# Optimization experiments

Hardware: AMD Instinct MI355X
Metric: run time of the kernel (lower is better)

Reference implementation:

```python
import jax, jax.numpy as jnp
import numpy as np

THRESH = 1.0
TAU_M = 20.0
TAU_S = 5.0
NUM_STEPS = 8
SCALE = 0.2
BATCH = 8
DM = np.float32(np.exp(-1.0 / TAU_M))
DS = np.float32(np.exp(-1.0 / TAU_S))


@jax.custom_vjp
def spike_fn(x):
    return (x > 0.0).astype(x.dtype)

def _sf_fwd(x):
    return (x > 0.0).astype(x.dtype), x

def _sf_bwd(x, g):
    # rectangular surrogate gradient (lens = 0.5), standard for NOSO/SNN training
    return (g * (jnp.abs(x) < 0.5).astype(x.dtype),)

spike_fn.defvjp(_sf_fwd, _sf_bwd)


def conv5x5(x, w):
    return jax.lax.conv_general_dilated(x, w, (1, 1), ((2, 2), (2, 2)),
                                        dimension_numbers=('NCHW', 'OIHW', 'NCHW'))


def noso_conv(w, in_sp, sav, vm, vs):
    # dual-exponential NOSO neuron: pre-synaptic traces vm/vs, membrane u = sav*(conv(vm)-conv(vs))
    vm = DM * vm + in_sp
    vs = DS * vs + in_sp
    um = conv5x5(vm, w)
    us = conv5x5(vs, w)
    u = sav * (um - us)
    sp = spike_fn(u - THRESH)
    sav = sav * (1.0 - sp)  # one spike per neuron
    return sav, vm, vs, um, u, sp


def noso_fc(w, in_sp, sav, vm, vs):
    vm = DM * vm + in_sp
    vs = DS * vs + in_sp
    um = jnp.einsum('bi,oi->bo', vm, w)
    us = jnp.einsum('bi,oi->bo', vs, w)
    u = sav * (um - us)
    sp = spike_fn(u - THRESH)
    sav = sav * (1.0 - sp)
    return sav, vm, vs, um, u, sp


def minpool(sp, lat):
    # latency-based 2x2 min-pool: pass through the spike whose neuron fired earliest
    b, c, h, w = sp.shape
    s = sp.reshape(b, c, h // 2, 2, w // 2, 2).transpose(0, 1, 2, 4, 3, 5).reshape(b, c, h // 2, w // 2, 4)
    l = lat.reshape(b, c, h // 2, 2, w // 2, 2).transpose(0, 1, 2, 4, 3, 5).reshape(b, c, h // 2, w // 2, 4)
    idx = jnp.argmin(l, axis=-1)
    return jnp.take_along_axis(s, idx[..., None], axis=-1)[..., 0]


def xavier(key, shape, fan_in, fan_out):
    a = np.float32(np.sqrt(6.0 / (fan_in + fan_out)))
    return jax.random.uniform(key, shape, jnp.float32, -a, a)


def setup_inputs():
    key = jax.random.key(0)
    ks = jax.random.split(key, 9)
    inp = {'input': jax.random.uniform(ks[0], (BATCH, 3, 32, 32), jnp.float32)}
    def cw(k, o, i):
        return xavier(k, (o, i, 5, 5), i * 25, o * 25)
    def lw(k, o, i):
        return xavier(k, (o, i), i, o)
    inp['wc1'] = cw(ks[1], 64, 3)
    inp['wc2'] = cw(ks[2], 128, 64)
    inp['wc3'] = cw(ks[3], 256, 128)
    inp['wc4'] = cw(ks[4], 512, 256)
    inp['wc5'] = cw(ks[5], 256, 512)
    inp['wf1'] = lw(ks[6], 1024, 16384)
    inp['wf2'] = lw(ks[7], 512, 1024)
    inp['wf3'] = lw(ks[8], 10, 512)
    inp['batch_size'] = BATCH
    return inp


def forward(input, wc1, wc2, wc3, wc4, wc5, wf1, wf2, wf3, batch_size):
    B = batch_size
    f32 = jnp.float32
    def Z(*s):
        return jnp.zeros((B,) + s, f32)
    def O(*s):
        return jnp.ones((B,) + s, f32)
    carry = {
        'in_u': Z(3, 32, 32),
        'h1': (O(64, 32, 32), Z(3, 32, 32), Z(3, 32, 32)),
        'h2': (O(128, 32, 32), Z(64, 32, 32), Z(64, 32, 32)),
        'h3': (O(256, 16, 16), Z(128, 16, 16), Z(128, 16, 16)),
        'h4': (O(512, 8, 8), Z(256, 8, 8), Z(256, 8, 8)),
        'h5': (O(256, 8, 8), Z(512, 8, 8), Z(512, 8, 8)),
        'f1': (O(1024), Z(16384), Z(16384)),
        'f2': (O(512), Z(1024), Z(1024)),
        'f3': (O(10), Z(512), Z(512)),
        'p1e': Z(128, 32, 32),
        'p1l': float(NUM_STEPS) * O(128, 32, 32),
        'p2e': Z(256, 16, 16),
        'p2l': float(NUM_STEPS) * O(256, 16, 16),
        'te': Z(10),
        'out_t': float(NUM_STEPS) * O(10),
        'out_u': Z(10),
        'sum_sp': jnp.zeros((9,), f32),
    }

    def step(c, _):
        # input encoding neuron (thresh=1, leaky integrate + reset on spike)
        in_u = DM * c['in_u'] + input * SCALE
        in_sp = spike_fn(in_u - 1.0)
        in_u = in_u * (1.0 - in_sp)
        s1, vm1, vs1, um1, u1, sp1 = noso_conv(wc1, in_sp, *c['h1'])
        s2, vm2, vs2, um2, u2, sp2 = noso_conv(wc2, sp1, *c['h2'])
        p1e = c['p1e'] + ((c['p1e'] + (um2 != 0).astype(f32)) != 0).astype(f32)
        p1l = c['p1l'] + jax.lax.stop_gradient(sp2) * (p1e - NUM_STEPS + 1.0)
        s3, vm3, vs3, um3, u3, sp3 = noso_conv(wc3, minpool(sp2, p1l), *c['h3'])
        p2e = c['p2e'] + ((c['p2e'] + (um3 != 0).astype(f32)) != 0).astype(f32)
        p2l = c['p2l'] + jax.lax.stop_gradient(sp3) * (p2e - NUM_STEPS + 1.0)
        s4, vm4, vs4, um4, u4, sp4 = noso_conv(wc4, minpool(sp3, p2l), *c['h4'])
        s5, vm5, vs5, um5, u5, sp5 = noso_conv(wc5, sp4, *c['h5'])
        sf1, vmf1, vsf1, umf1, uf1, spf1 = noso_fc(wf1, sp5.reshape(B, -1), *c['f1'])
        sf2, vmf2, vsf2, umf2, uf2, spf2 = noso_fc(wf2, spf1, *c['f2'])
        sf3, vmf3, vsf3, umf3, uf3, spf3 = noso_fc(wf3, spf2, *c['f3'])
        te = c['te'] + ((c['te'] + (uf3 != 0).astype(f32)) != 0).astype(f32)
        out_t = c['out_t'] + spf3 * jax.lax.stop_gradient(te - NUM_STEPS)  # dodt forward
        out_u = c['out_u'] + spf3 * uf3
        sum_sp = c['sum_sp'] + jnp.stack([in_sp.sum(), sp1.sum(), sp2.sum(), sp3.sum(),
                                          sp4.sum(), sp5.sum(), spf1.sum(), spf2.sum(), spf3.sum()])
        nc = {'in_u': in_u,
              'h1': (s1, vm1, vs1), 'h2': (s2, vm2, vs2), 'h3': (s3, vm3, vs3),
              'h4': (s4, vm4, vs4), 'h5': (s5, vm5, vs5),
              'f1': (sf1, vmf1, vsf1), 'f2': (sf2, vmf2, vsf2), 'f3': (sf3, vmf3, vsf3),
              'p1e': p1e, 'p1l': p1l, 'p2e': p2e, 'p2l': p2l,
              'te': te, 'out_t': out_t, 'out_u': out_u, 'sum_sp': sum_sp}
        return nc, None

    c, _ = jax.lax.scan(step, carry, None, length=NUM_STEPS)
    return c['out_t'], c['out_u'], c['sum_sp']


def reference(input, wc1, wc2, wc3, wc4, wc5, wf1, wf2, wf3, batch_size):
    return forward(input, wc1, wc2, wc3, wc4, wc5, wf1, wf2, wf3, batch_size)
```

## Files before the change

kernel.cpp:

```cpp
#include <hip/hip_runtime.h>
#include <cstddef>

#define B 8
constexpr int TAIL_NB = 256;

constexpr float DM = 0.95122942450071400910f;
constexpr float DS = 0.81873075307798185867f;

constexpr int BS_L0 = 3 * 32 * 32;
constexpr int BS_L1 = 64 * 32 * 32;
constexpr int BS_P1 = 128 * 16 * 16;
constexpr int BS_P2 = 256 * 8 * 8;
constexpr int BS_L4 = 512 * 8 * 8;
constexpr int BS_L5 = 256 * 8 * 8;
constexpr int BS_F1 = 1024;
constexpr int BS_F2 = 512;

constexpr size_t I_L1 = 0;
constexpr size_t I_P1 = I_L1 + 8 * (size_t)B * BS_L1;
constexpr size_t I_P2 = I_P1 + 8 * (size_t)B * BS_P1;
constexpr size_t I_L4 = I_P2 + 8 * (size_t)B * BS_P2;
constexpr size_t I_L5 = I_L4 + 8 * (size_t)B * BS_L4;
constexpr size_t I_F1 = I_L5 + 8 * (size_t)B * BS_L5;
constexpr size_t I_F2 = I_F1 + 8 * (size_t)B * BS_F1;
constexpr size_t I_CNT = I_F2 + 8 * (size_t)B * BS_F2;
constexpr size_t I_SUMP = I_CNT + 512;
constexpr size_t I_BAR = I_SUMP + 16;
constexpr size_t INT_TOTAL = I_BAR + 2;
constexpr size_t WS_NEED = INT_TOTAL * sizeof(int);

constexpr int ilog2(int n) { int l = 0; while (n > 1) { n >>= 1; ++l; } return l; }

__device__ __forceinline__ int ldcnt(const int* p) {
  return __hip_atomic_load(p, __ATOMIC_RELAXED, __HIP_MEMORY_SCOPE_AGENT);
}

__device__ __forceinline__ void block_stage(bool sp, int idx, int* s_list, int* s_n) {
  unsigned long long bal = __ballot(sp);
  if (bal == 0ull) return;
  int lane = threadIdx.x & 63;
  int leader = (int)__ffsll((unsigned long long)bal) - 1;
  int base = 0;
  if (lane == leader) base = atomicAdd(s_n, __popcll(bal));
  base = __shfl(base, leader);
  if (sp) s_list[base + __popcll(bal & ((1ull << lane) - 1ull))] = idx;
}

__device__ __forceinline__ void wave_append(bool sp, int idx, int* cnt, int* list) {
  unsigned long long bal = __ballot(sp);
  if (bal == 0ull) return;
  int lane = threadIdx.x & 63;
  int leader = (int)__ffsll((unsigned long long)bal) - 1;
  int base = 0;
  if (lane == leader) base = atomicAdd(cnt, __popcll(bal));
  base = __shfl(base, leader);
  if (sp) list[base + __popcll(bal & ((1ull << lane) - 1ull))] = idx;
}

__device__ __forceinline__ bool layer_any(const int* cnt, int ci, int tid, int* s_gate) {
  __syncthreads();
  if (tid == 0) *s_gate = 0;
  __syncthreads();
  if (tid < 64) {
    int t = tid >> 3, b = tid & 7;
    if (ldcnt(cnt + (t * 8 + ci) * 8 + b) > 0) *s_gate = 1;
  }
  __syncthreads();
  return *s_gate != 0;
}

__device__ __forceinline__ void gbar(int* bar, int tid) {
  __threadfence();
  __syncthreads();
  if (tid == 0) {
    int g = __hip_atomic_load(bar + 1, __ATOMIC_RELAXED, __HIP_MEMORY_SCOPE_AGENT);
    int a = __hip_atomic_fetch_add(bar, 1, __ATOMIC_ACQ_REL, __HIP_MEMORY_SCOPE_AGENT);
    if (a == TAIL_NB - 1) {
      __hip_atomic_store(bar, 0, __ATOMIC_RELAXED, __HIP_MEMORY_SCOPE_AGENT);
      __hip_atomic_store(bar + 1, g + 1, __ATOMIC_RELEASE, __HIP_MEMORY_SCOPE_AGENT);
    } else {
      while (__hip_atomic_load(bar + 1, __ATOMIC_ACQUIRE, __HIP_MEMORY_SCOPE_AGENT) == g)
        __builtin_amdgcn_s_sleep(1);
    }
  }
  __syncthreads();
  __threadfence();
}

__global__ void k_init(int* __restrict__ cw) {
  if (threadIdx.x < 530) cw[threadIdx.x] = 0;
}

__global__ __launch_bounds__(512) void k_conv1_enc(const float* __restrict__ in,
                                                   const float* __restrict__ w,
                                                   int* __restrict__ cnt,
                                                   int* __restrict__ out_list0) {
  const int tid = threadIdx.x;
  const int plane = blockIdx.x;
  const int b = plane >> 6;
  const int oc = plane & 63;
  __shared__ float s_w[75];
  __shared__ float s_acc[1024];
  __shared__ int s_list[BS_L0];
  __shared__ int s_n;
  if (tid < 75) s_w[tid] = w[oc * 75 + tid];
  float x[6], u[6];
#pragma unroll
  for (int k = 0; k < 6; ++k) {
    x[k] = in[b * BS_L0 + tid + k * 512] * 0.2f;
    u[k] = 0.0f;
  }
  float um[2], us[2], sav[2];
#pragma unroll
  for (int k = 0; k < 2; ++k) { um[k] = 0.0f; us[k] = 0.0f; sav[k] = 1.0f; }
  bool active = false;
#pragma clang loop unroll(disable)
  for (int t = 0; t < 8; ++t) {
    if (tid == 0) s_n = 0;
    __syncthreads();
#pragma unroll
    for (int k = 0; k < 6; ++k) {
      u[k] = DM * u[k] + x[k];
      bool sp = (u[k] - 1.0f > 0.0f);
      if (sp) u[k] = 0.0f;
      block_stage(sp, tid + k * 512, s_list, &s_n);
    }
    __syncthreads();
    const int Sin = s_n;
    if (oc == 0 && tid == 0) cnt[(t * 8 + 0) * 8 + b] = Sin;
    active = active || (Sin > 0);
    if (!active) continue;
#pragma clang loop unroll(disable)
    for (int p = tid; p < 1024; p += 512) s_acc[p] = 0.0f;
    __syncthreads();
    const int total = Sin << 5;
#pragma clang loop unroll(disable)
    for (int i = tid; i < total; i += 512) {
      int k = i & 31;
      if (k < 25) {
        int loc = s_list[i >> 5];
        int c = loc >> 10;
        int p = loc & 1023;
        int ki = (k * 205) >> 10;
        int oy = (p >> 5) + 2 - ki;
        int ox = (p & 31) + 2 - (k - ki * 5);
        if ((unsigned)oy < 32u && (unsigned)ox < 32u)
          atomicAdd(&s_acc[(oy << 5) + ox], s_w[c * 25 + k]);
      }
    }
    __syncthreads();
    int* out_cnt = cnt + (t * 8 + 1) * 8 + b;
    int* out_list = out_list0 + ((size_t)t * B + b) * BS_L1;
#pragma unroll
    for (int k = 0; k < 2; ++k) {
      int p = tid + k * 512;
      float cv = s_acc[p];
      float m = DM * um[k] + cv;
      float s2 = DS * us[k] + cv;
      um[k] = m;
      us[k] = s2;
      float uu = sav[k] * (m - s2);
      bool sp = (uu - 1.0f > 0.0f);
      if (sp) sav[k] = 0.0f;
      wave_append(sp, (oc << 10) + p, out_cnt, out_list);
    }
    __syncthreads();
  }
}

template <int CIN, int COUT, int H, int W, bool POOL, int PPB, bool WLDS>
__device__ void conv_phase(int bid, int tid, const float* __restrict__ w, int* cnt, int in_ci,
                           int out_ci, const int* __restrict__ in_list0, int in_bs,
                           int* __restrict__ out_list0, int out_bs, float* sump_layer,
                           float* s_acc, float* s_plb, float* s_spb, float* s_w, int* s_list,
                           int* s_n, int* s_base, int* s_uc, int* s_cnt) {
  constexpr int HW = H * W;
  constexpr int HWlog = ilog2(HW);
  constexpr int Wlog = ilog2(W);
  constexpr int PPT = (HW + 255) / 256;
  int wcount = 0;
  const int b = (bid * PPB) >> ilog2(COUT);
  if (tid < 8) s_cnt[tid] = ldcnt(cnt + (tid * 8 + in_ci) * 8 + b);
  __syncthreads();
#pragma clang loop unroll(disable)
  for (int pl = 0; pl < PPB; ++pl) {
    const int plane = bid * PPB + pl;
    const int oc = plane & (COUT - 1);
    if constexpr (WLDS) {
#pragma clang loop unroll(disable)
      for (int j = tid; j < CIN * 25; j += 256) s_w[j] = w[(size_t)oc * CIN * 25 + j];
    }
    float um[PPT], us[PPT], sav[PPT], pe[PPT], plat[PPT];
#pragma unroll
    for (int k = 0; k < PPT; ++k) {
      um[k] = 0.0f; us[k] = 0.0f; sav[k] = 1.0f; pe[k] = 0.0f; plat[k] = 8.0f;
    }
    bool active = false;
#pragma clang loop unroll(disable)
    for (int t = 0; t < 8; ++t) {
      const int S = s_cnt[t];
      if (!active && S == 0) continue;
      active = true;
#pragma clang loop unroll(disable)
      for (int p = tid; p < HW; p += 256) s_acc[p] = 0.0f;
      if (tid == 0) *s_n = 0;
      __syncthreads();
      const int* list = in_list0 + ((size_t)t * B + b) * in_bs;
#pragma clang loop unroll(disable)
      for (int s = tid; s < S; s += 256) {
        int loc = list[s];
        int c = loc >> HWlog;
        int p = loc & (HW - 1);
        int y = p >> Wlog, x = p & (W - 1);
        const float* wp = WLDS ? (const float*)s_w + c * 25 : w + ((size_t)oc * CIN + c) * 25;
#pragma clang loop unroll(disable)
        for (int ki = 0; ki < 5; ++ki) {
          int oy = y + 2 - ki;
          if ((unsigned)oy < (unsigned)H) {
#pragma clang loop unroll(disable)
            for (int kj = 0; kj < 5; ++kj) {
              int ox = x + 2 - kj;
              if ((unsigned)ox < (unsigned)W) atomicAdd(&s_acc[oy * W + ox], wp[ki * 5 + kj]);
            }
          }
        }
      }
      __syncthreads();
#pragma unroll
      for (int k = 0; k < PPT; ++k) {
        int p = tid + k * 256;
        bool lane_ok = (p < HW);
        float cv = lane_ok ? s_acc[p] : 0.0f;
        float m = DM * um[k] + cv;
        float s2 = DS * us[k] + cv;
        um[k] = m;
        us[k] = s2;
        float uu = sav[k] * (m - s2);
        bool sp = lane_ok && (uu - 1.0f > 0.0f);
        if (sp) sav[k] = 0.0f;
        if constexpr (POOL) {
          unsigned long long bal = __ballot(sp);
          if ((tid & 63) == 0) wcount += (int)__popcll(bal);
          if (lane_ok) {
            float act = (m != 0.0f) ? 1.0f : 0.0f;
            float pen = pe[k] + (((pe[k] + act) != 0.0f) ? 1.0f : 0.0f);
            pe[k] = pen;
            if (sp) plat[k] += pen - 7.0f;
            s_plb[p] = plat[k];
            s_spb[p] = sp ? 1.0f : 0.0f;
          }
        } else {
          block_stage(sp, (oc << HWlog) + p, s_list, s_n);
        }
      }
      __syncthreads();
      if constexpr (POOL) {
        constexpr int HP = H / 2, WP = W / 2;
#pragma clang loop unroll(disable)
        for (int q = tid; q < HP * WP; q += 256) {
          int py = q / WP, px = q - py * WP;
          int base = (2 * py) * W + 2 * px;
          float l0 = s_plb[base], l1 = s_plb[base + 1], l2 = s_plb[base + W],
                l3 = s_plb[base + W + 1];
          int off = 0;
          float lm = l0;
          if (l1 < lm) { lm = l1; off = 1; }
          if (l2 < lm) { lm = l2; off = W; }
          if (l3 < lm) { lm = l3; off = W + 1; }
          bool psp = (s_spb[base + off] != 0.0f);
          block_stage(psp, oc * (HP * WP) + q, s_list, s_n);
        }
        __syncthreads();
      }
      if (tid == 0 && *s_n > 0) *s_base = atomicAdd(cnt + (t * 8 + out_ci) * 8 + b, *s_n);
      __syncthreads();
      int* out_list = out_list0 + ((size_t)t * B + b) * out_bs;
      int n = *s_n;
#pragma clang loop unroll(disable)
      for (int j = tid; j < n; j += 256) out_list[*s_base + j] = s_list[j];
      __syncthreads();
    }
  }
  if constexpr (POOL) {
    if (tid == 0) *s_uc = 0;
    __syncthreads();
    if ((tid & 63) == 0 && wcount) atomicAdd(s_uc, wcount);
    __syncthreads();
    if (tid == 0 && *s_uc) atomicAdd(sump_layer + b, (float)*s_uc);
  }
}

template <int IN, int OUT>
__device__ void fc_phase(int bid, int tid, const float* __restrict__ w, int* cnt, int in_ci,
                         int out_ci, const int* __restrict__ in_list0, int in_bs,
                         int* __restrict__ out_list0, int out_bs, int* s_list, int* s_n,
                         int* s_base, int* s_cnt) {
  const int q = bid * 256 + tid;
  const int b = q >> ilog2(OUT);
  const int o = q & (OUT - 1);
  if (tid < 8) s_cnt[tid] = ldcnt(cnt + (tid * 8 + in_ci) * 8 + b);
  __syncthreads();
  float um = 0.0f, us = 0.0f, sav = 1.0f;
  bool active = false;
#pragma clang loop unroll(disable)
  for (int t = 0; t < 8; ++t) {
    const int S = s_cnt[t];
    if (!active && S == 0) continue;
    active = true;
    if (tid == 0) *s_n = 0;
    __syncthreads();
    const int* list = in_list0 + ((size_t)t * B + b) * in_bs;
    float acc = 0.0f;
#pragma clang loop unroll(disable)
    for (int s = 0; s < S; ++s) acc += w[(size_t)o * IN + list[s]];
    float m = DM * um + acc;
    float s2 = DS * us + acc;
    um = m;
    us = s2;
    float uu = sav * (m - s2);
    bool sp = (uu - 1.0f > 0.0f);
    if (sp) sav = 0.0f;
    block_stage(sp, o, s_list, s_n);
    __syncthreads();
    if (tid == 0 && *s_n > 0) *s_base = atomicAdd(cnt + (t * 8 + out_ci) * 8 + b, *s_n);
    __syncthreads();
    int* out_list = out_list0 + ((size_t)t * B + b) * out_bs;
    int n = *s_n;
#pragma clang loop unroll(disable)
    for (int j = tid; j < n; j += 256) out_list[*s_base + j] = s_list[j];
    __syncthreads();
  }
}

__device__ void fc3_phase(int tid, const float* __restrict__ w, const int* cnt, int in_ci,
                          const int* __restrict__ in_list0, int in_bs,
                          const float* __restrict__ sump, float* __restrict__ out, int* s_c3) {
  if (tid == 0) *s_c3 = 0;
  __syncthreads();
  const bool lane_ok = (tid < 80);
  const int b = lane_ok ? tid / 10 : 0;
  const int o = lane_ok ? tid - b * 10 : 0;
  float um = 0.0f, us = 0.0f, sav = 1.0f, te = 0.0f, ot = 8.0f, ou = 0.0f;
  bool active = false;
#pragma clang loop unroll(disable)
  for (int t = 0; t < 8; ++t) {
    const int S = lane_ok ? ldcnt(cnt + (t * 8 + in_ci) * 8 + b) : 0;
    if (!active && !__any(S > 0)) continue;
    active = true;
    const int* list = in_list0 + ((size_t)t * B + b) * in_bs;
    float acc = 0.0f;
#pragma clang loop unroll(disable)
    for (int s = 0; s < S; ++s) acc += w[o * 512 + list[s]];
    float m = DM * um + acc;
    float s2 = DS * us + acc;
    um = m;
    us = s2;
    float uu = sav * (m - s2);
    bool sp = lane_ok && (uu - 1.0f > 0.0f);
    if (sp) sav = 0.0f;
    float act = (uu != 0.0f) ? 1.0f : 0.0f;
    te = te + (((te + act) != 0.0f) ? 1.0f : 0.0f);
    if (sp) {
      ot += te - 8.0f;
      ou += uu;
    }
    unsigned long long bal = __ballot(sp);
    if ((tid & 63) == 0 && bal) atomicAdd(s_c3, (int)__popcll(bal));
  }
  if (tid < 80) {
    out[tid] = ot;
    out[80 + tid] = ou;
  }
  __syncthreads();
  if (tid < 8) {
    float s = 0.0f;
    if (tid == 2 || tid == 3) {
      const float* sp = sump + (tid - 2) * 8;
      for (int b2 = 0; b2 < 8; ++b2) s += sp[b2];
    } else {
      for (int t = 0; t < 8; ++t)
        for (int b2 = 0; b2 < 8; ++b2) s += (float)cnt[(t * 8 + tid) * 8 + b2];
    }
    out[160 + tid] = s;
  }
  if (tid == 0) out[168] = (float)*s_c3;
}

__global__ __launch_bounds__(256) void k_tail(const float* __restrict__ wc2,
                                              const float* __restrict__ wc3,
                                              const float* __restrict__ wc4,
                                              const float* __restrict__ wc5,
                                              const float* __restrict__ wf1,
                                              const float* __restrict__ wf2,
                                              const float* __restrict__ wf3,
                                              float* __restrict__ out, int* __restrict__ iws) {
  __shared__ float s_w[3200];
  __shared__ float s_acc[1024];
  __shared__ float s_plb[1024];
  __shared__ float s_spb[1024];
  __shared__ int s_list[1024];
  __shared__ int s_n, s_base, s_uc, s_gate, s_c3, s_cnt[8];
  const int tid = threadIdx.x;
  const int bid = blockIdx.x;
  int* cnt = iws + I_CNT;
  float* sump = (float*)(iws + I_SUMP);
  int* bar = iws + I_BAR;

  if (layer_any(cnt, 1, tid, &s_gate)) {
    conv_phase<64, 128, 32, 32, true, 4, true>(bid, tid, wc2, cnt, 1, 2, iws + I_L1, BS_L1,
                                               iws + I_P1, BS_P1, sump + 0, s_acc, s_plb, s_spb,
                                               s_w, s_list, &s_n, &s_base, &s_uc, s_cnt);
    gbar(bar, tid);
  }
  if (layer_any(cnt, 2, tid, &s_gate)) {
    conv_phase<128, 256, 16, 16, true, 8, true>(bid, tid, wc3, cnt, 2, 3, iws + I_P1, BS_P1,
                                                iws + I_P2, BS_P2, sump + 8, s_acc, s_plb, s_spb,
                                                s_w, s_list, &s_n, &s_base, &s_uc, s_cnt);
    gbar(bar, tid);
  }
  if (layer_any(cnt, 3, tid, &s_gate)) {
    conv_phase<256, 512, 8, 8, false, 16, false>(bid, tid, wc4, cnt, 3, 4, iws + I_P2, BS_P2,
                                                 iws + I_L4, BS_L4, nullptr, s_acc, s_plb, s_spb,
                                                 s_w, s_list, &s_n, &s_base, &s_uc, s_cnt);
    gbar(bar, tid);
  }
  if (layer_any(cnt, 4, tid, &s_gate)) {
    conv_phase<512, 256, 8, 8, false, 8, false>(bid, tid, wc5, cnt, 4, 5, iws + I_L4, BS_L4,
                                                iws + I_L5, BS_L5, nullptr, s_acc, s_plb, s_spb,
                                                s_w, s_list, &s_n, &s_base, &s_uc, s_cnt);
    gbar(bar, tid);
  }
  if (layer_any(cnt, 5, tid, &s_gate)) {
    if (bid < B * 1024 / 256)
      fc_phase<16384, 1024>(bid, tid, wf1, cnt, 5, 6, iws + I_L5, BS_L5, iws + I_F1, BS_F1,
                            s_list, &s_n, &s_base, s_cnt);
    gbar(bar, tid);
  }
  if (layer_any(cnt, 6, tid, &s_gate)) {
    if (bid < B * 512 / 256)
      fc_phase<1024, 512>(bid, tid, wf2, cnt, 6, 7, iws + I_F1, BS_F1, iws + I_F2, BS_F2,
                          s_list, &s_n, &s_base, s_cnt);
    gbar(bar, tid);
  }
  if (bid == 0)
    fc3_phase(tid, wf3, cnt, 7, iws + I_F2, BS_F2, sump, out, &s_c3);
}

extern "C" void kernel_launch(void* const* d_in, const int* in_sizes, int n_in, void* d_out,
                              int out_size, void* d_ws, size_t ws_size, hipStream_t stream) {
  const float* input = (const float*)d_in[0];
  const float* wc1 = (const float*)d_in[1];
  const float* wc2 = (const float*)d_in[2];
  const float* wc3 = (const float*)d_in[3];
  const float* wc4 = (const float*)d_in[4];
  const float* wc5 = (const float*)d_in[5];
  const float* wf1 = (const float*)d_in[6];
  const float* wf2 = (const float*)d_in[7];
  const float* wf3 = (const float*)d_in[8];
  float* out = (float*)d_out;
  int* iws = (int*)d_ws;
  if (ws_size < WS_NEED) return;

  k_init<<<1, 530, 0, stream>>>(iws + I_CNT);
  k_conv1_enc<<<512, 512, 0, stream>>>(input, wc1, iws + I_CNT, iws + I_L1);
  k_tail<<<TAIL_NB, 256, 0, stream>>>(wc2, wc3, wc4, wc5, wf1, wf2, wf3, out, iws);
}
```

Before: 71.59 us.

## Split input spike encoding into a per-image kernel shared by conv1 blocks

Input spike encoding was recomputed by every output-channel block; it now runs once per batch image in a dedicated kernel. That kernel compacts spikes with wave ballots and a prefix scan, writes the lists to global memory, and zeroes the counters in place of the old init kernel. The conv1 kernel loads the precomputed lists and uses 256-thread blocks. This removes redundant encoding and shared-memory atomics, at the cost of an extra global round trip and a kernel dependency.

```diff
diff --git a/kernel.cpp b/kernel.cpp
--- a/kernel.cpp
+++ b/kernel.cpp
@@ -16,7 +16,8 @@
 constexpr int BS_F1 = 1024;
 constexpr int BS_F2 = 512;
 
-constexpr size_t I_L1 = 0;
+constexpr size_t I_L0 = 0;
+constexpr size_t I_L1 = I_L0 + 8 * (size_t)B * BS_L0;
 constexpr size_t I_P1 = I_L1 + 8 * (size_t)B * BS_L1;
 constexpr size_t I_P2 = I_P1 + 8 * (size_t)B * BS_P1;
 constexpr size_t I_L4 = I_P2 + 8 * (size_t)B * BS_P2;
@@ -87,55 +88,94 @@
   __threadfence();
 }
 
-__global__ void k_init(int* __restrict__ cw) {
-  if (threadIdx.x < 530) cw[threadIdx.x] = 0;
-}
-
-__global__ __launch_bounds__(512) void k_conv1_enc(const float* __restrict__ in,
-                                                   const float* __restrict__ w,
-                                                   int* __restrict__ cnt,
-                                                   int* __restrict__ out_list0) {
+__global__ __launch_bounds__(512) void k_encode(const float* __restrict__ in,
+                                                int* __restrict__ iws) {
+  const int tid = threadIdx.x;
+  const int b = blockIdx.x;
+  int* cnt = iws + I_CNT;
+  if (tid < 56) {
+    int t = tid / 7, ci = 1 + tid % 7;
+    cnt[(t * 8 + ci) * 8 + b] = 0;
+  }
+  if (b == 0 && tid >= 64 && tid < 82) iws[I_SUMP + (tid - 64)] = 0;
+  __shared__ unsigned long long s_bal[48];
+  __shared__ int s_off[48];
+  const int lane = tid & 63, w = tid >> 6;
+  float x[6], u[6];
+#pragma unroll
+  for (int k = 0; k < 6; ++k) {
+    x[k] = in[b * BS_L0 + tid + k * 512] * 0.2f;
+    u[k] = 0.0f;
+  }
+#pragma clang loop unroll(disable)
+  for (int t = 0; t < 8; ++t) {
+    __syncthreads();
+    int spm = 0;
+#pragma unroll
+    for (int k = 0; k < 6; ++k) {
+      u[k] = DM * u[k] + x[k];
+      bool sp = (u[k] - 1.0f > 0.0f);
+      if (sp) { u[k] = 0.0f; spm |= 1 << k; }
+      unsigned long long bal = __ballot(sp);
+      if (lane == 0) s_bal[k * 8 + w] = bal;
+    }
+    __syncthreads();
+    if (tid < 48) {
+      int v = __popcll(s_bal[tid]);
+      int incl = v;
+#pragma unroll
+      for (int d = 1; d < 64; d <<= 1) {
+        int o = __shfl_up(incl, d);
+        if (lane >= d) incl += o;
+      }
+      s_off[tid] = incl - v;
+      if (tid == 47) cnt[(t * 8 + 0) * 8 + b] = incl;
+    }
+    __syncthreads();
+    int* list = iws + I_L0 + ((size_t)t * B + b) * BS_L0;
+#pragma unroll
+    for (int k = 0; k < 6; ++k) {
+      if (spm & (1 << k)) {
+        int word = k * 8 + w;
+        int rank = __popcll(s_bal[word] & ((1ull << lane) - 1ull));
+        list[s_off[word] + rank] = tid + k * 512;
+      }
+    }
+  }
+}
+
+__global__ __launch_bounds__(256) void k_conv1(const float* __restrict__ w,
+                                               int* __restrict__ iws) {
   const int tid = threadIdx.x;
   const int plane = blockIdx.x;
   const int b = plane >> 6;
   const int oc = plane & 63;
+  int* cnt = iws + I_CNT;
   __shared__ float s_w[75];
   __shared__ float s_acc[1024];
   __shared__ int s_list[BS_L0];
-  __shared__ int s_n;
-  if (tid < 75) s_w[tid] = w[oc * 75 + tid];
-  float x[6], u[6];
-#pragma unroll
-  for (int k = 0; k < 6; ++k) {
-    x[k] = in[b * BS_L0 + tid + k * 512] * 0.2f;
-    u[k] = 0.0f;
-  }
-  float um[2], us[2], sav[2];
-#pragma unroll
-  for (int k = 0; k < 2; ++k) { um[k] = 0.0f; us[k] = 0.0f; sav[k] = 1.0f; }
+  __shared__ int s_cnt[8];
+  if (tid < 8) s_cnt[tid] = ldcnt(cnt + (tid * 8 + 0) * 8 + b);
+  if (tid >= 64 && tid < 139) s_w[tid - 64] = w[oc * 75 + (tid - 64)];
+  __syncthreads();
+  float um[4], us[4], sav[4];
+#pragma unroll
+  for (int k = 0; k < 4; ++k) { um[k] = 0.0f; us[k] = 0.0f; sav[k] = 1.0f; }
   bool active = false;
 #pragma clang loop unroll(disable)
   for (int t = 0; t < 8; ++t) {
-    if (tid == 0) s_n = 0;
-    __syncthreads();
-#pragma unroll
-    for (int k = 0; k < 6; ++k) {
-      u[k] = DM * u[k] + x[k];
-      bool sp = (u[k] - 1.0f > 0.0f);
-      if (sp) u[k] = 0.0f;
-      block_stage(sp, tid + k * 512, s_list, &s_n);
-    }
-    __syncthreads();
-    const int Sin = s_n;
-    if (oc == 0 && tid == 0) cnt[(t * 8 + 0) * 8 + b] = Sin;
-    active = active || (Sin > 0);
-    if (!active) continue;
-#pragma clang loop unroll(disable)
-    for (int p = tid; p < 1024; p += 512) s_acc[p] = 0.0f;
-    __syncthreads();
-    const int total = Sin << 5;
-#pragma clang loop unroll(disable)
-    for (int i = tid; i < total; i += 512) {
+    const int S = s_cnt[t];
+    if (!active && S == 0) continue;
+    active = true;
+#pragma clang loop unroll(disable)
+    for (int p = tid; p < 1024; p += 256) s_acc[p] = 0.0f;
+    const int* glist = iws + I_L0 + ((size_t)t * B + b) * BS_L0;
+#pragma clang loop unroll(disable)
+    for (int j = tid; j < S; j += 256) s_list[j] = glist[j];
+    __syncthreads();
+    const int total = S << 5;
+#pragma clang loop unroll(disable)
+    for (int i = tid; i < total; i += 256) {
       int k = i & 31;
       if (k < 25) {
         int loc = s_list[i >> 5];
@@ -150,10 +190,10 @@
     }
     __syncthreads();
     int* out_cnt = cnt + (t * 8 + 1) * 8 + b;
-    int* out_list = out_list0 + ((size_t)t * B + b) * BS_L1;
-#pragma unroll
-    for (int k = 0; k < 2; ++k) {
-      int p = tid + k * 512;
+    int* out_list = iws + I_L1 + ((size_t)t * B + b) * BS_L1;
+#pragma unroll
+    for (int k = 0; k < 4; ++k) {
+      int p = tid + (k << 8);
       float cv = s_acc[p];
       float m = DM * um[k] + cv;
       float s2 = DS * us[k] + cv;
@@ -461,7 +501,7 @@
   int* iws = (int*)d_ws;
   if (ws_size < WS_NEED) return;
 
-  k_init<<<1, 530, 0, stream>>>(iws + I_CNT);
-  k_conv1_enc<<<512, 512, 0, stream>>>(input, wc1, iws + I_CNT, iws + I_L1);
+  k_encode<<<B, 512, 0, stream>>>(input, iws);
+  k_conv1<<<512, 256, 0, stream>>>(wc1, iws);
   k_tail<<<TAIL_NB, 256, 0, stream>>>(wc2, wc3, wc4, wc5, wf1, wf2, wf3, out, iws);
 }
```

Result: slower. 74.17 us (+3.6%).
